# Kernel optimization log

Measured on AMD Instinct MI355X. Metric: run time of the kernel, lower is better.

The kernel has to match this reference:

```python
import jax, jax.numpy as jnp
import numpy as np

N, C, D = 16384, 1000, 1024

def setup_inputs() -> dict:
    key = jax.random.key(0)
    k1, k2 = jax.random.split(key)
    embedding = jax.random.normal(k1, (N, D), dtype=jnp.float32)
    # nn.Parameter init is zeros in the module, but zeros give degenerate (all-equal)
    # distances; use random centers as a trained-parameter stand-in.
    centers = jax.random.normal(k2, (C, D), dtype=jnp.float32)
    return {"embedding": embedding, "centers": centers}

def reference(embedding, centers):
    # pytorch_ood.utils.pairwise_distances: squared Euclidean via norm + matmul trick
    x_norm = jnp.sum(embedding * embedding, axis=1, keepdims=True)      # [N, 1]
    y_norm = jnp.sum(centers * centers, axis=1)[None, :]                # [1, C]
    dist = x_norm + y_norm - 2.0 * jnp.matmul(embedding, centers.T)     # [N, C]
    return jnp.maximum(dist, 0.0)
```

## Files before the change

### kernel.cpp

```cpp
#include <hip/hip_runtime.h>
#include <hip/hip_bf16.h>
#include <stdint.h>

#define N_ROWS 16384
#define C_ROWS 1000
#define C_PAD  1024
#define D_DIM  1024

#define BM 128
#define BN 128
#define BK 32
#define KSTEPS (D_DIM / BK)
#define TILE_ELEMS (BM * BK)

typedef __attribute__((ext_vector_type(8))) short    bf16x8;
typedef __attribute__((ext_vector_type(4))) float    f32x4;
typedef __attribute__((ext_vector_type(4))) uint32_t u32x4;

__device__ __forceinline__ uint32_t pk2bf(float lo, float hi) {
    union { float f; uint32_t u; } a, b;
    a.f = lo; b.f = hi;
    uint32_t l = (a.u + 0x8000u) >> 16;
    uint32_t h = (b.u + 0x8000u) >> 16;
    return l | (h << 16);
}

__device__ __forceinline__ void gl_lds16(const uint16_t* g, uint16_t* l) {
    __builtin_amdgcn_global_load_lds(
        (const __attribute__((address_space(1))) void*)g,
        (__attribute__((address_space(3))) void*)l,
        16, 0, 0);
}

__device__ __forceinline__ void conv_row(const float* __restrict__ x,
                                         uint16_t* __restrict__ xt,
                                         float* __restrict__ norms,
                                         int wid, int lane, bool valid) {
    const int tile = wid >> 7;
    const int row  = wid & 127;
    uint16_t* tbase = xt + (size_t)tile * KSTEPS * TILE_ELEMS;
    const int kslot = lane & 3;
    const int cellb = (kslot * 128 + row) * 8;
    if (valid) {
        const f32x4* rp = (const f32x4*)(x + (size_t)wid * D_DIM);
        float s = 0.f;
#pragma unroll
        for (int i = 0; i < 2; ++i) {
            f32x4 v0 = rp[i * 128 + lane * 2];
            f32x4 v1 = rp[i * 128 + lane * 2 + 1];
            s += v0[0]*v0[0] + v0[1]*v0[1] + v0[2]*v0[2] + v0[3]*v0[3]
               + v1[0]*v1[0] + v1[1]*v1[1] + v1[2]*v1[2] + v1[3]*v1[3];
            u32x4 p;
            p[0] = pk2bf(v0[0], v0[1]); p[1] = pk2bf(v0[2], v0[3]);
            p[2] = pk2bf(v1[0], v1[1]); p[3] = pk2bf(v1[2], v1[3]);
            const int t = i * 16 + (lane >> 2);
            *(u32x4*)(tbase + (size_t)t * TILE_ELEMS + cellb) = p;
        }
#pragma unroll
        for (int off = 32; off > 0; off >>= 1) s += __shfl_down(s, off, 64);
        if (lane == 0) norms[wid] = s;
    } else {
        u32x4 z = {0, 0, 0, 0};
#pragma unroll
        for (int i = 0; i < 2; ++i) {
            const int t = i * 16 + (lane >> 2);
            *(u32x4*)(tbase + (size_t)t * TILE_ELEMS + cellb) = z;
        }
        if (lane == 0) norms[wid] = 0.f;
    }
}

__global__ void convert_norm_both(const float* __restrict__ E,
                                  uint16_t* __restrict__ Et,
                                  float* __restrict__ xn,
                                  const float* __restrict__ Cc,
                                  uint16_t* __restrict__ Ct,
                                  float* __restrict__ yn) {
    int wid  = (blockIdx.x * blockDim.x + threadIdx.x) >> 6;
    int lane = threadIdx.x & 63;
    if (wid < N_ROWS) {
        conv_row(E, Et, xn, wid, lane, true);
    } else {
        int w2 = wid - N_ROWS;
        conv_row(Cc, Ct, yn, w2, lane, w2 < C_ROWS);
    }
}

__global__ __launch_bounds__(256, 4)
void dist_gemm2(const uint16_t* __restrict__ At,
                const uint16_t* __restrict__ Bt,
                const float* __restrict__ xn,
                const float* __restrict__ yn,
                float* __restrict__ out) {
    __shared__ uint16_t As[2][TILE_ELEMS];
    __shared__ uint16_t Bs[2][TILE_ELEMS];

    const int tid  = threadIdx.x;
    const int lane = tid & 63;
    const int wid  = tid >> 6;
    const int wm   = wid >> 1;
    const int wn   = wid & 1;

    const int rowTile = blockIdx.x;
    const int colTile = blockIdx.y;

    const uint16_t* Abase = At + (size_t)rowTile * KSTEPS * TILE_ELEMS;
    const uint16_t* Bbase = Bt + (size_t)colTile * KSTEPS * TILE_ELEMS;

    const int off0 = tid * 8;
    const int off1 = 2048 + tid * 8;

    const int fA = ((lane >> 4) * 128 + wm * 64 + (lane & 15)) * 8;
    const int fB = ((lane >> 4) * 128 + wn * 64 + (lane & 15)) * 8;

    f32x4 acc[4][4];
#pragma unroll
    for (int m = 0; m < 4; ++m)
#pragma unroll
        for (int n = 0; n < 4; ++n) acc[m][n] = (f32x4)(0.f);

#define STAGE(buf, t)                                               \
    do {                                                            \
        const uint16_t* ga = Abase + (size_t)(t) * TILE_ELEMS;      \
        const uint16_t* gb = Bbase + (size_t)(t) * TILE_ELEMS;      \
        gl_lds16(ga + off0, &As[buf][off0]);                        \
        gl_lds16(ga + off1, &As[buf][off1]);                        \
        gl_lds16(gb + off0, &Bs[buf][off0]);                        \
        gl_lds16(gb + off1, &Bs[buf][off1]);                        \
    } while (0)

    STAGE(0, 0);
    __syncthreads();

    int cur = 0;
    for (int t = 0; t < KSTEPS; ++t) {
        if (t + 1 < KSTEPS) STAGE(cur ^ 1, t + 1);
        bf16x8 ar[4], br[4];
#pragma unroll
        for (int m = 0; m < 4; ++m) ar[m] = *(const bf16x8*)&As[cur][fA + m * 16 * 8];
#pragma unroll
        for (int n = 0; n < 4; ++n) br[n] = *(const bf16x8*)&Bs[cur][fB + n * 16 * 8];
#pragma unroll
        for (int m = 0; m < 4; ++m)
#pragma unroll
            for (int n = 0; n < 4; ++n)
                acc[m][n] = __builtin_amdgcn_mfma_f32_16x16x32_bf16(
                    ar[m], br[n], acc[m][n], 0, 0, 0);
        __syncthreads();
        cur ^= 1;
    }
#undef STAGE

    float* Cs = (float*)&As[0][0];
    const int mrow = (lane >> 4) * 4;
    const int ccol = wn * 64 + (lane & 15);
    const int srow = tid >> 4;
    const int scol = (tid & 15) * 4;

#pragma unroll
    for (int p = 0; p < 8; ++p) {
        __syncthreads();
        if (wm == (p >> 2)) {
            const int m = p & 3;
#pragma unroll
            for (int n = 0; n < 4; ++n)
#pragma unroll
                for (int r = 0; r < 4; ++r)
                    Cs[(mrow + r) * 132 + ccol + n * 16] = acc[m][n][r];
        }
        __syncthreads();
        const int grow = rowTile * BM + p * 16 + srow;
        const float xr = xn[grow];
        float* orow = out + (size_t)grow * C_ROWS;
#pragma unroll
        for (int s = 0; s < 2; ++s) {
            const int c  = scol + s * 64;
            const int gc = colTile * BN + c;
            f32x4 d = *(f32x4*)&Cs[srow * 132 + c];
            f32x4 y4 = *(const f32x4*)&yn[gc];
            f32x4 v;
#pragma unroll
            for (int j = 0; j < 4; ++j)
                v[j] = fmaxf(xr + y4[j] - 2.0f * d[j], 0.f);
            if (gc + 3 < C_ROWS) {
                *(f32x4*)&orow[gc] = v;
            } else {
#pragma unroll
                for (int j = 0; j < 4; ++j)
                    if (gc + j < C_ROWS) orow[gc + j] = v[j];
            }
        }
    }
}

__global__ void row_norms_kernel(const float* __restrict__ x,
                                 float* __restrict__ out,
                                 int rows, int pad_rows) {
    int gid  = blockIdx.x * blockDim.x + threadIdx.x;
    int wid  = gid >> 6;
    int lane = threadIdx.x & 63;
    if (wid >= pad_rows) return;
    float s = 0.f;
    if (wid < rows) {
        const f32x4* rp = (const f32x4*)(x + (size_t)wid * D_DIM);
#pragma unroll
        for (int r = 0; r < D_DIM / 256; ++r) {
            f32x4 v = rp[r * 64 + lane];
            s += v[0]*v[0] + v[1]*v[1] + v[2]*v[2] + v[3]*v[3];
        }
    }
#pragma unroll
    for (int off = 32; off > 0; off >>= 1) s += __shfl_down(s, off, 64);
    if (lane == 0) out[wid] = s;
}

__global__ __launch_bounds__(256, 2)
void dist_gemm_kernel(const float* __restrict__ E,
                      const float* __restrict__ Cc,
                      const float* __restrict__ xn,
                      const float* __restrict__ yn,
                      float* __restrict__ out) {
    __shared__ uint16_t As[4 * 128 * 8];
    __shared__ uint16_t Bs[4 * 128 * 8];
    const int tid  = threadIdx.x;
    const int lane = tid & 63;
    const int wid  = tid >> 6;
    const int wm   = wid >> 1;
    const int wn   = wid & 1;
    const int rowTile = blockIdx.y;
    const int colTile = blockIdx.x;
    const int srow = tid & 127;
    const int sp   = tid >> 7;
    const int ga = rowTile * 128 + srow;
    const int gb = colTile * 128 + srow;
    const float* Arow = E  + (size_t)ga * D_DIM + sp * 16;
    const float* Brow = Cc + (size_t)gb * D_DIM + sp * 16;
    const bool bvalid = (gb < C_ROWS);
    f32x4 acc[4][4];
#pragma unroll
    for (int m = 0; m < 4; ++m)
#pragma unroll
        for (int n = 0; n < 4; ++n) acc[m][n] = (f32x4)(0.f);
    const int fragA_base = (((lane >> 4) * 128) + wm * 64 + (lane & 15)) * 8;
    const int fragB_base = (((lane >> 4) * 128) + wn * 64 + (lane & 15)) * 8;
    const int stA0 = ((sp * 2) * 128 + srow) * 8;
    const int stA1 = ((sp * 2 + 1) * 128 + srow) * 8;
    for (int k0 = 0; k0 < D_DIM; k0 += 32) {
        f32x4 a0 = *(const f32x4*)(Arow + k0);
        f32x4 a1 = *(const f32x4*)(Arow + k0 + 4);
        f32x4 a2 = *(const f32x4*)(Arow + k0 + 8);
        f32x4 a3 = *(const f32x4*)(Arow + k0 + 12);
        f32x4 b0 = (f32x4)(0.f), b1 = (f32x4)(0.f),
              b2 = (f32x4)(0.f), b3 = (f32x4)(0.f);
        if (bvalid) {
            b0 = *(const f32x4*)(Brow + k0);
            b1 = *(const f32x4*)(Brow + k0 + 4);
            b2 = *(const f32x4*)(Brow + k0 + 8);
            b3 = *(const f32x4*)(Brow + k0 + 12);
        }
        u32x4 pa01, pa23, pb01, pb23;
        pa01[0] = pk2bf(a0[0], a0[1]); pa01[1] = pk2bf(a0[2], a0[3]);
        pa01[2] = pk2bf(a1[0], a1[1]); pa01[3] = pk2bf(a1[2], a1[3]);
        pa23[0] = pk2bf(a2[0], a2[1]); pa23[1] = pk2bf(a2[2], a2[3]);
        pa23[2] = pk2bf(a3[0], a3[1]); pa23[3] = pk2bf(a3[2], a3[3]);
        pb01[0] = pk2bf(b0[0], b0[1]); pb01[1] = pk2bf(b0[2], b0[3]);
        pb01[2] = pk2bf(b1[0], b1[1]); pb01[3] = pk2bf(b1[2], b1[3]);
        pb23[0] = pk2bf(b2[0], b2[1]); pb23[1] = pk2bf(b2[2], b2[3]);
        pb23[2] = pk2bf(b3[0], b3[1]); pb23[3] = pk2bf(b3[2], b3[3]);
        __syncthreads();
        *(u32x4*)&As[stA0] = pa01;
        *(u32x4*)&As[stA1] = pa23;
        *(u32x4*)&Bs[stA0] = pb01;
        *(u32x4*)&Bs[stA1] = pb23;
        __syncthreads();
        bf16x8 ar[4], br[4];
#pragma unroll
        for (int m = 0; m < 4; ++m) ar[m] = *(const bf16x8*)&As[fragA_base + m * 16 * 8];
#pragma unroll
        for (int n = 0; n < 4; ++n) br[n] = *(const bf16x8*)&Bs[fragB_base + n * 16 * 8];
#pragma unroll
        for (int m = 0; m < 4; ++m)
#pragma unroll
            for (int n = 0; n < 4; ++n)
                acc[m][n] = __builtin_amdgcn_mfma_f32_16x16x32_bf16(
                    ar[m], br[n], acc[m][n], 0, 0, 0);
    }
    const int orow0 = rowTile * 128 + wm * 64 + ((lane >> 4) * 4);
    const int ocol0 = colTile * 128 + wn * 64 + (lane & 15);
#pragma unroll
    for (int n = 0; n < 4; ++n) {
        int gc = ocol0 + n * 16;
        if (gc >= C_ROWS) continue;
        float ynv = yn[gc];
#pragma unroll
        for (int m = 0; m < 4; ++m) {
            int gr = orow0 + m * 16;
#pragma unroll
            for (int r = 0; r < 4; ++r) {
                float v = xn[gr + r] + ynv - 2.0f * acc[m][n][r];
                out[(size_t)(gr + r) * C_ROWS + gc] = fmaxf(v, 0.f);
            }
        }
    }
}

extern "C" void kernel_launch(void* const* d_in, const int* in_sizes, int n_in,
                              void* d_out, int out_size, void* d_ws, size_t ws_size,
                              hipStream_t stream) {
    const float* E  = (const float*)d_in[0];
    const float* Cc = (const float*)d_in[1];
    float* out = (float*)d_out;

    uint16_t* Et = (uint16_t*)d_ws;
    uint16_t* Ct = Et + (size_t)N_ROWS * D_DIM;
    float*    xn = (float*)(Ct + (size_t)C_PAD * D_DIM);
    float*    yn = xn + N_ROWS;
    size_t need = (size_t)((char*)(yn + C_PAD) - (char*)d_ws);

    if (ws_size >= need) {
        convert_norm_both<<<(N_ROWS + C_PAD) / 4, 256, 0, stream>>>(
            E, Et, xn, Cc, Ct, yn);
        dim3 grid(N_ROWS / BM, C_PAD / BN);
        dist_gemm2<<<grid, 256, 0, stream>>>(Et, Ct, xn, yn, out);
    } else {
        float* fxn = (float*)d_ws;
        float* fyn = fxn + N_ROWS;
        row_norms_kernel<<<N_ROWS / 4, 256, 0, stream>>>(E,  fxn, N_ROWS, N_ROWS);
        row_norms_kernel<<<C_PAD  / 4, 256, 0, stream>>>(Cc, fyn, C_ROWS, C_PAD);
        dim3 grid(C_PAD / 128, N_ROWS / 128);
        dist_gemm_kernel<<<grid, 256, 0, stream>>>(E, Cc, fxn, fyn, out);
    }
}
```

Measured before the change: 65.18 us.

## Shrink GEMM column tile to 64 with a 64-row packed operand layout

Repacks both operands into 64-row k-major tiles and changes the distance GEMM to 128x64 output tiles. Each wave now computes a 64x32 sub-block, and the epilogue stride shrinks to match. The intent is to double the block count for better occupancy and CU fill, and to waste less work on the padded 1000→1024 columns. In exchange, arithmetic intensity per block drops, so more A-tile traffic and LDS loads are needed per MFMA.

```diff
diff --git a/kernel.cpp b/kernel.cpp
--- a/kernel.cpp
+++ b/kernel.cpp
@@ -8,10 +8,10 @@
 #define D_DIM  1024
 
 #define BM 128
-#define BN 128
+#define BN 64
 #define BK 32
 #define KSTEPS (D_DIM / BK)
-#define TILE_ELEMS (BM * BK)
+#define T64 2048
 
 typedef __attribute__((ext_vector_type(8))) short    bf16x8;
 typedef __attribute__((ext_vector_type(4))) float    f32x4;
@@ -36,11 +36,11 @@
                                          uint16_t* __restrict__ xt,
                                          float* __restrict__ norms,
                                          int wid, int lane, bool valid) {
-    const int tile = wid >> 7;
-    const int row  = wid & 127;
-    uint16_t* tbase = xt + (size_t)tile * KSTEPS * TILE_ELEMS;
+    const int tile = wid >> 6;
+    const int row  = wid & 63;
+    uint16_t* tbase = xt + (size_t)tile * KSTEPS * T64;
     const int kslot = lane & 3;
-    const int cellb = (kslot * 128 + row) * 8;
+    const int cellb = (kslot * 64 + row) * 8;
     if (valid) {
         const f32x4* rp = (const f32x4*)(x + (size_t)wid * D_DIM);
         float s = 0.f;
@@ -54,7 +54,7 @@
             p[0] = pk2bf(v0[0], v0[1]); p[1] = pk2bf(v0[2], v0[3]);
             p[2] = pk2bf(v1[0], v1[1]); p[3] = pk2bf(v1[2], v1[3]);
             const int t = i * 16 + (lane >> 2);
-            *(u32x4*)(tbase + (size_t)t * TILE_ELEMS + cellb) = p;
+            *(u32x4*)(tbase + (size_t)t * T64 + cellb) = p;
         }
 #pragma unroll
         for (int off = 32; off > 0; off >>= 1) s += __shfl_down(s, off, 64);
@@ -64,7 +64,7 @@
 #pragma unroll
         for (int i = 0; i < 2; ++i) {
             const int t = i * 16 + (lane >> 2);
-            *(u32x4*)(tbase + (size_t)t * TILE_ELEMS + cellb) = z;
+            *(u32x4*)(tbase + (size_t)t * T64 + cellb) = z;
         }
         if (lane == 0) norms[wid] = 0.f;
     }
@@ -87,13 +87,13 @@
 }
 
 __global__ __launch_bounds__(256, 4)
-void dist_gemm2(const uint16_t* __restrict__ At,
+void dist_gemm6(const uint16_t* __restrict__ At,
                 const uint16_t* __restrict__ Bt,
                 const float* __restrict__ xn,
                 const float* __restrict__ yn,
                 float* __restrict__ out) {
-    __shared__ uint16_t As[2][TILE_ELEMS];
-    __shared__ uint16_t Bs[2][TILE_ELEMS];
+    __shared__ uint16_t As[2][2 * T64];
+    __shared__ uint16_t Bs[2][T64];
 
     const int tid  = threadIdx.x;
     const int lane = tid & 63;
@@ -104,29 +104,26 @@
     const int rowTile = blockIdx.x;
     const int colTile = blockIdx.y;
 
-    const uint16_t* Abase = At + (size_t)rowTile * KSTEPS * TILE_ELEMS;
-    const uint16_t* Bbase = Bt + (size_t)colTile * KSTEPS * TILE_ELEMS;
-
-    const int off0 = tid * 8;
-    const int off1 = 2048 + tid * 8;
-
-    const int fA = ((lane >> 4) * 128 + wm * 64 + (lane & 15)) * 8;
-    const int fB = ((lane >> 4) * 128 + wn * 64 + (lane & 15)) * 8;
-
-    f32x4 acc[4][4];
+    const uint16_t* A0 = At + (size_t)(2 * rowTile)     * KSTEPS * T64;
+    const uint16_t* A1 = A0 + (size_t)KSTEPS * T64;
+    const uint16_t* Bb = Bt + (size_t)colTile           * KSTEPS * T64;
+
+    const int so = tid * 8;
+
+    const int fA = ((lane >> 4) * 64 + (lane & 15)) * 8;
+    const int fB = ((lane >> 4) * 64 + wn * 32 + (lane & 15)) * 8;
+
+    f32x4 acc[4][2];
 #pragma unroll
     for (int m = 0; m < 4; ++m)
 #pragma unroll
-        for (int n = 0; n < 4; ++n) acc[m][n] = (f32x4)(0.f);
+        for (int n = 0; n < 2; ++n) acc[m][n] = (f32x4)(0.f);
 
 #define STAGE(buf, t)                                               \
     do {                                                            \
-        const uint16_t* ga = Abase + (size_t)(t) * TILE_ELEMS;      \
-        const uint16_t* gb = Bbase + (size_t)(t) * TILE_ELEMS;      \
-        gl_lds16(ga + off0, &As[buf][off0]);                        \
-        gl_lds16(ga + off1, &As[buf][off1]);                        \
-        gl_lds16(gb + off0, &Bs[buf][off0]);                        \
-        gl_lds16(gb + off1, &Bs[buf][off1]);                        \
+        gl_lds16(A0 + (size_t)(t) * T64 + so, &As[buf][so]);        \
+        gl_lds16(A1 + (size_t)(t) * T64 + so, &As[buf][T64 + so]);  \
+        gl_lds16(Bb + (size_t)(t) * T64 + so, &Bs[buf][so]);        \
     } while (0)
 
     STAGE(0, 0);
@@ -135,15 +132,16 @@
     int cur = 0;
     for (int t = 0; t < KSTEPS; ++t) {
         if (t + 1 < KSTEPS) STAGE(cur ^ 1, t + 1);
-        bf16x8 ar[4], br[4];
-#pragma unroll
-        for (int m = 0; m < 4; ++m) ar[m] = *(const bf16x8*)&As[cur][fA + m * 16 * 8];
-#pragma unroll
-        for (int n = 0; n < 4; ++n) br[n] = *(const bf16x8*)&Bs[cur][fB + n * 16 * 8];
+        const uint16_t* Ab = &As[cur][wm * T64];
+        bf16x8 ar[4], br[2];
+#pragma unroll
+        for (int m = 0; m < 4; ++m) ar[m] = *(const bf16x8*)(Ab + fA + m * 16 * 8);
+#pragma unroll
+        for (int n = 0; n < 2; ++n) br[n] = *(const bf16x8*)(&Bs[cur][fB + n * 16 * 8]);
 #pragma unroll
         for (int m = 0; m < 4; ++m)
 #pragma unroll
-            for (int n = 0; n < 4; ++n)
+            for (int n = 0; n < 2; ++n)
                 acc[m][n] = __builtin_amdgcn_mfma_f32_16x16x32_bf16(
                     ar[m], br[n], acc[m][n], 0, 0, 0);
         __syncthreads();
@@ -153,7 +151,7 @@
 
     float* Cs = (float*)&As[0][0];
     const int mrow = (lane >> 4) * 4;
-    const int ccol = wn * 64 + (lane & 15);
+    const int ccol = wn * 32 + (lane & 15);
     const int srow = tid >> 4;
     const int scol = (tid & 15) * 4;
 
@@ -163,32 +161,28 @@
         if (wm == (p >> 2)) {
             const int m = p & 3;
 #pragma unroll
-            for (int n = 0; n < 4; ++n)
+            for (int n = 0; n < 2; ++n)
 #pragma unroll
                 for (int r = 0; r < 4; ++r)
-                    Cs[(mrow + r) * 132 + ccol + n * 16] = acc[m][n][r];
+                    Cs[(mrow + r) * 68 + ccol + n * 16] = acc[m][n][r];
         }
         __syncthreads();
         const int grow = rowTile * BM + p * 16 + srow;
         const float xr = xn[grow];
         float* orow = out + (size_t)grow * C_ROWS;
-#pragma unroll
-        for (int s = 0; s < 2; ++s) {
-            const int c  = scol + s * 64;
-            const int gc = colTile * BN + c;
-            f32x4 d = *(f32x4*)&Cs[srow * 132 + c];
-            f32x4 y4 = *(const f32x4*)&yn[gc];
-            f32x4 v;
+        const int gc = colTile * BN + scol;
+        f32x4 d = *(f32x4*)&Cs[srow * 68 + scol];
+        f32x4 y4 = *(const f32x4*)&yn[gc];
+        f32x4 v;
+#pragma unroll
+        for (int j = 0; j < 4; ++j)
+            v[j] = fmaxf(xr + y4[j] - 2.0f * d[j], 0.f);
+        if (gc + 3 < C_ROWS) {
+            *(f32x4*)&orow[gc] = v;
+        } else {
 #pragma unroll
             for (int j = 0; j < 4; ++j)
-                v[j] = fmaxf(xr + y4[j] - 2.0f * d[j], 0.f);
-            if (gc + 3 < C_ROWS) {
-                *(f32x4*)&orow[gc] = v;
-            } else {
-#pragma unroll
-                for (int j = 0; j < 4; ++j)
-                    if (gc + j < C_ROWS) orow[gc + j] = v[j];
-            }
+                if (gc + j < C_ROWS) orow[gc + j] = v[j];
         }
     }
 }
@@ -321,7 +315,7 @@
         convert_norm_both<<<(N_ROWS + C_PAD) / 4, 256, 0, stream>>>(
             E, Et, xn, Cc, Ct, yn);
         dim3 grid(N_ROWS / BM, C_PAD / BN);
-        dist_gemm2<<<grid, 256, 0, stream>>>(Et, Ct, xn, yn, out);
+        dist_gemm6<<<grid, 256, 0, stream>>>(Et, Ct, xn, yn, out);
     } else {
         float* fxn = (float*)d_ws;
         float* fyn = fxn + N_ROWS;
```

Result: slower. 75.33 us (+15.6%).
